# Kernel tuning notes

Measured on AMD Instinct MI355X. Metric: run time of the kernel, lower is better.

The kernel has to match this reference:

```python
import jax, jax.numpy as jnp
import numpy as np

NH = 32      # num_attention_heads
HD = 128     # head dim (kv_channels)
NG = 2       # multi_query_group_num
LAYER_NUMBER = 1


def apply_rotary_pos_emb(x, rope_cache):
    # x: [b, np, sq, hn]; rope_cache: [1, sq_max, rot/2, 2]
    b, nh, sq, hn = x.shape
    rot_dim = rope_cache.shape[-2] * 2
    xr, x_pass = x[..., :rot_dim], x[..., rot_dim:]
    xs = xr.reshape(b, nh, sq, rot_dim // 2, 2)
    c = rope_cache[:, :sq].reshape(-1, 1, sq, rot_dim // 2, 2)
    out = jnp.stack(
        [xs[..., 0] * c[..., 0] - xs[..., 1] * c[..., 1],
         xs[..., 1] * c[..., 0] + xs[..., 0] * c[..., 1]], axis=-1)
    out = out.reshape(b, nh, sq, rot_dim)
    return jnp.concatenate([out, x_pass], axis=-1)


def setup_inputs() -> dict:
    key = jax.random.key(0)
    ks = jax.random.split(key, 5)
    b, sq, h = 2, 2048, 4096
    qkv_out = NH * HD + 2 * NG * HD  # 4608
    return {
        "hidden_states": jax.random.normal(ks[0], (b, sq, h), jnp.float32),
        "rope_cache": jax.random.normal(ks[1], (1, sq, HD // 4, 2), jnp.float32),
        "W_qkv": jax.random.normal(ks[2], (h, qkv_out), jnp.float32) * 0.02,
        "b_qkv": jax.random.normal(ks[3], (qkv_out,), jnp.float32) * 0.02,
        "W_dense": jax.random.normal(ks[4], (NH * HD, h), jnp.float32) * 0.02,
    }


def reference(hidden_states, rope_cache, W_qkv, b_qkv, W_dense):
    b, sq, h = hidden_states.shape
    mixed = hidden_states @ W_qkv + b_qkv  # [b, sq, nh*hd + 2*ng*hd]
    q_sz = NH * HD
    kv_sz = NG * HD
    q = mixed[..., :q_sz].reshape(b, sq, NH, HD).transpose(0, 2, 1, 3)          # [b,nh,sq,hd]
    k = mixed[..., q_sz:q_sz + kv_sz].reshape(b, sq, NG, HD).transpose(0, 2, 1, 3)  # [b,ng,sq,hd]
    v = mixed[..., q_sz + kv_sz:].reshape(b, sq, NG, HD).transpose(0, 2, 1, 3)      # [b,ng,sq,hd]

    q = apply_rotary_pos_emb(q, rope_cache)
    k = apply_rotary_pos_emb(k, rope_cache)

    # expand KV groups to full heads (multi-query attention)
    rep = NH // NG
    k = jnp.broadcast_to(k[:, :, None], (b, NG, rep, sq, HD)).reshape(b, NH, sq, HD)
    v = jnp.broadcast_to(v[:, :, None], (b, NG, rep, sq, HD)).reshape(b, NH, sq, HD)

    # CoreAttention (eager path, fp32 softmax, causal)
    coeff = float(max(1, LAYER_NUMBER))  # apply_query_key_layer_scaling
    norm_factor = np.sqrt(HD) * coeff
    scores = jnp.einsum("bhqd,bhkd->bhqk", q, k) / norm_factor
    scores = scores.astype(jnp.float32) * coeff
    causal = jnp.tril(jnp.ones((sq, sq), dtype=bool))
    scores = jnp.where(causal[None, None], scores, -jnp.inf)
    probs = jax.nn.softmax(scores, axis=-1).astype(v.dtype)
    context = jnp.einsum("bhqk,bhkd->bhqd", probs, v)   # [b,nh,sq,hd]
    context = context.transpose(0, 2, 1, 3).reshape(b, sq, NH * HD)
    return context @ W_dense
```

## Files before the change

kernel.cpp:

```cpp
#include <hip/hip_runtime.h>
#include <hip/hip_bf16.h>
#include <stdint.h>

#define B_    2
#define SQ    2048
#define H_    4096
#define NHEAD 32
#define HDIM  128
#define NGRP  2
#define QKVN  4608
#define SCALE 0.08838834764831845f
#define QSCALE (0.08838834764831845f * 1.4426950408889634f)

typedef __attribute__((ext_vector_type(8))) short bf16x8;
typedef __attribute__((ext_vector_type(4))) short bf16x4;
typedef __attribute__((ext_vector_type(4))) float f32x4;

__device__ __forceinline__ float b2f(short s) {
  union { float f; unsigned u; } x; x.u = ((unsigned)(unsigned short)s) << 16; return x.f;
}
__device__ __forceinline__ short f2b(float f) {
  union { float f; unsigned u; } x; x.f = f;
  unsigned r = x.u + 0x7fffu + ((x.u >> 16) & 1u);
  return (short)(r >> 16);
}
__device__ __forceinline__ void gll16(const void* g, void* l) {
  __builtin_amdgcn_global_load_lds(
      (const __attribute__((address_space(1))) unsigned int*)g,
      (__attribute__((address_space(3))) unsigned int*)l, 16, 0, 0);
}

__global__ void conv_f32_bf16(const float* __restrict__ x, short* __restrict__ y, int n) {
  int i = (blockIdx.x * blockDim.x + threadIdx.x) * 4;
  if (i >= n) return;
  float4 v = *(const float4*)(x + i);
  union { short s[4]; uint2 u; } o;
  o.s[0] = f2b(v.x); o.s[1] = f2b(v.y); o.s[2] = f2b(v.z); o.s[3] = f2b(v.w);
  *(uint2*)(y + i) = o.u;
}

__global__ void transpose_f32_bf16(const float* __restrict__ W, short* __restrict__ Wt,
                                   int R, int C) {
  __shared__ float tile[32][33];
  int c0 = blockIdx.x * 32, r0 = blockIdx.y * 32;
  int tx = threadIdx.x, ty = threadIdx.y;
  #pragma unroll
  for (int i = 0; i < 32; i += 8)
    tile[ty + i][tx] = W[(size_t)(r0 + ty + i) * C + c0 + tx];
  __syncthreads();
  #pragma unroll
  for (int i = 0; i < 32; i += 8)
    Wt[(size_t)(c0 + ty + i) * R + r0 + tx] = f2b(tile[tx][ty + i]);
}

template<bool BIAS, bool OUTF32>
__global__ __launch_bounds__(256, 2) void gemm_bf16(
    const short* __restrict__ A, const short* __restrict__ Bt,
    const float* __restrict__ bias, short* __restrict__ outb,
    float* __restrict__ outf, int M, int N, int K)
{
  __shared__ short smA[128 * 64];
  __shared__ short smB[128 * 64];
  const int t = threadIdx.x;
  const int l = t & 63;
  const int w = t >> 6;
  const int wr = w >> 1, wc = w & 1;
  const int m0 = blockIdx.y * 128, n0 = blockIdx.x * 128;

  const f32x4 z = {0.f, 0.f, 0.f, 0.f};
  f32x4 acc[4][4];
  #pragma unroll
  for (int m = 0; m < 4; ++m)
    #pragma unroll
    for (int n = 0; n < 4; ++n) acc[m][n] = z;

  for (int k0 = 0; k0 < K; k0 += 64) {
    __syncthreads();
    #pragma unroll
    for (int i = 0; i < 4; ++i) {
      int c = t + i * 256;
      int row = c >> 3, slot = c & 7;
      int ss = slot ^ (row & 7);
      gll16(A  + (size_t)(m0 + row) * K + k0 + ss * 8,
            (char*)smA + (i * 256 + w * 64) * 16);
      gll16(Bt + (size_t)(n0 + row) * K + k0 + ss * 8,
            (char*)smB + (i * 256 + w * 64) * 16);
    }
    __syncthreads();
    #pragma unroll
    for (int kk = 0; kk < 2; ++kk) {
      bf16x8 a[4], b[4];
      #pragma unroll
      for (int m = 0; m < 4; ++m) {
        int row = wr * 64 + m * 16 + (l & 15);
        int off = (kk * 64 + ((l >> 4) << 4)) ^ ((row & 7) << 4);
        a[m] = *(const bf16x8*)((const char*)smA + row * 128 + off);
      }
      #pragma unroll
      for (int n = 0; n < 4; ++n) {
        int row = wc * 64 + n * 16 + (l & 15);
        int off = (kk * 64 + ((l >> 4) << 4)) ^ ((row & 7) << 4);
        b[n] = *(const bf16x8*)((const char*)smB + row * 128 + off);
      }
      #pragma unroll
      for (int m = 0; m < 4; ++m)
        #pragma unroll
        for (int n = 0; n < 4; ++n)
          acc[m][n] = __builtin_amdgcn_mfma_f32_16x16x32_bf16(a[m], b[n], acc[m][n], 0, 0, 0);
    }
  }

  #pragma unroll
  for (int m = 0; m < 4; ++m) {
    int row = m0 + wr * 64 + m * 16 + ((l >> 4) << 2);
    #pragma unroll
    for (int n = 0; n < 4; ++n) {
      int col = n0 + wc * 64 + n * 16 + (l & 15);
      float bv = BIAS ? bias[col] : 0.f;
      #pragma unroll
      for (int j = 0; j < 4; ++j) {
        float vv = acc[m][n][j] + bv;
        if (OUTF32) outf[(size_t)(row + j) * N + col] = vv;
        else        outb[(size_t)(row + j) * N + col] = f2b(vv);
      }
    }
  }
}

__global__ __launch_bounds__(512, 2) void gemm256(
    const short* __restrict__ A, const short* __restrict__ Bt,
    float* __restrict__ outf, int M, int N, int K, int nbx)
{
  __shared__ char sm[131072];
  const int t = threadIdx.x, l = t & 63, w = t >> 6;
  const int lq = l & 15, hi = l >> 4;
  const int wm = w >> 2, wn = w & 3;
  const int nwg = (int)gridDim.x;
  const int oid = (int)blockIdx.x;
  const int swz = (oid & 7) * (nwg >> 3) + (oid >> 3);
  const int by = swz / nbx, bx = swz - by * nbx;
  const int m0 = by * 256, n0 = bx * 256;
  const int nkt = K >> 6;

  auto stage = [&](int tt, int u) {
    int kb = (tt < nkt ? tt : tt - nkt) << 6;
    char* buf = sm + ((tt & 1) << 16);
    #pragma unroll
    for (int i = 0; i < 2; ++i) {
      int c = (i << 9) + t;
      int grow = (u < 2) ? (c >> 3) + ((u & 1) << 7)
                         : (c >> 3) + (i << 6) + ((u & 1) << 6);
      int ss = (c & 7) ^ (grow & 7);
      const short* src = (u < 2) ? Bt + (size_t)(n0 + grow) * K + kb + ss * 8
                                 : A  + (size_t)(m0 + grow) * K + kb + ss * 8;
      gll16(src, buf + (u < 2 ? 32768 : 0) + grow * 128 + (c & 7) * 16);
    }
  };

  bf16x8 aC[2][2], bC[4][2];
  auto ldA = [&](int b, int q) {
    #pragma unroll
    for (int fr = 0; fr < 2; ++fr) {
      int ra = wm * 128 + q * 32 + fr * 16 + lq;
      #pragma unroll
      for (int kk = 0; kk < 2; ++kk)
        aC[fr][kk] = *(const bf16x8*)(sm + (b << 16) + ra * 128 + (((kk << 2) + hi) ^ (ra & 7)) * 16);
    }
  };
  auto ldB = [&](int b) {
    #pragma unroll
    for (int fc = 0; fc < 4; ++fc) {
      int rb = wn * 64 + fc * 16 + lq;
      #pragma unroll
      for (int kk = 0; kk < 2; ++kk)
        bC[fc][kk] = *(const bf16x8*)(sm + (b << 16) + 32768 + rb * 128 + (((kk << 2) + hi) ^ (rb & 7)) * 16);
    }
  };

  const f32x4 z = {0.f, 0.f, 0.f, 0.f};
  f32x4 acc[8][4];
  #pragma unroll
  for (int i = 0; i < 8; ++i)
    #pragma unroll
    for (int j = 0; j < 4; ++j) acc[i][j] = z;

  stage(0, 0); stage(0, 1); stage(0, 2); stage(0, 3);
  asm volatile("s_waitcnt vmcnt(0)" ::: "memory");
  __builtin_amdgcn_s_barrier();

#define GPHASE(Q, VM)                                                     \
  {                                                                       \
    if ((Q) == 0) ldB(bsel);                                              \
    ldA(bsel, (Q));                                                       \
    stage(T + 1, (Q));                                                    \
    __builtin_amdgcn_s_barrier();                                         \
    __builtin_amdgcn_s_setprio(1);                                        \
    _Pragma("unroll")                                                     \
    for (int kk = 0; kk < 2; ++kk)                                        \
      _Pragma("unroll")                                                   \
      for (int fr = 0; fr < 2; ++fr)                                      \
        _Pragma("unroll")                                                 \
        for (int fc = 0; fc < 4; ++fc)                                    \
          acc[(Q) * 2 + fr][fc] = __builtin_amdgcn_mfma_f32_16x16x32_bf16(\
              aC[fr][kk], bC[fc][kk], acc[(Q) * 2 + fr][fc], 0, 0, 0);    \
    __builtin_amdgcn_s_setprio(0);                                        \
    if ((VM) == 4) asm volatile("s_waitcnt vmcnt(4)" ::: "memory");       \
    if ((VM) == 2) asm volatile("s_waitcnt vmcnt(2)" ::: "memory");       \
    __builtin_amdgcn_s_barrier();                                         \
  }

  for (int T = 0; T < nkt; ++T) {
    const int bsel = T & 1;
    GPHASE(0, -1)
    GPHASE(1, 4)
    GPHASE(2, -1)
    GPHASE(3, 2)
  }
#undef GPHASE

  #pragma unroll
  for (int q = 0; q < 4; ++q)
    #pragma unroll
    for (int fr = 0; fr < 2; ++fr) {
      int gr0 = m0 + wm * 128 + q * 32 + fr * 16 + hi * 4;
      #pragma unroll
      for (int fc = 0; fc < 4; ++fc) {
        int col = n0 + wn * 64 + fc * 16 + lq;
        #pragma unroll
        for (int j = 0; j < 4; ++j)
          outf[(size_t)(gr0 + j) * N + col] = acc[q * 2 + fr][fc][j];
      }
    }
}

__global__ void rope_split(const short* __restrict__ mixed, const float* __restrict__ rope,
                           short* __restrict__ qo, short* __restrict__ ko, short* __restrict__ vo)
{
  const int CH = QKVN / 8;
  int idx = blockIdx.x * blockDim.x + threadIdx.x;
  if (idx >= B_ * SQ * CH) return;
  int row = idx / CH;
  int cc = (idx - row * CH) * 8;
  int b = row >> 11, s = row & 2047;

  bf16x8 xv = *(const bf16x8*)(mixed + (size_t)row * QKVN + cc);
  float x[8];
  #pragma unroll
  for (int i = 0; i < 8; ++i) x[i] = b2f(xv[i]);

  int sect, hh, d = cc & 127;
  if (cc < 4096)      { sect = 0; hh = cc >> 7; }
  else if (cc < 4352) { sect = 1; hh = (cc - 4096) >> 7; }
  else                { sect = 2; hh = (cc - 4352) >> 7; }

  if (sect < 2 && d < 64) {
    float4 ca = *(const float4*)(rope + s * 64 + d);
    float4 cb = *(const float4*)(rope + s * 64 + d + 4);
    float t0;
    t0 = x[0]*ca.x - x[1]*ca.y; x[1] = x[1]*ca.x + x[0]*ca.y; x[0] = t0;
    t0 = x[2]*ca.z - x[3]*ca.w; x[3] = x[3]*ca.z + x[2]*ca.w; x[2] = t0;
    t0 = x[4]*cb.x - x[5]*cb.y; x[5] = x[5]*cb.x + x[4]*cb.y; x[4] = t0;
    t0 = x[6]*cb.z - x[7]*cb.w; x[7] = x[7]*cb.z + x[6]*cb.w; x[6] = t0;
  }
  if (sect == 0) {
    #pragma unroll
    for (int i = 0; i < 8; ++i) x[i] *= QSCALE;
  }

  short* dst; size_t oidx;
  if (sect == 0)      { dst = qo; oidx = (((size_t)(b * NHEAD + hh) * SQ) + s) * HDIM + d; }
  else if (sect == 1) { dst = ko; oidx = (((size_t)(b * NGRP + hh) * SQ) + s) * HDIM + d; }
  else                { dst = vo; oidx = (((size_t)(b * NGRP + hh) * SQ) + s) * HDIM + d; }
  bf16x8 ov;
  #pragma unroll
  for (int i = 0; i < 8; ++i) ov[i] = f2b(x[i]);
  *(bf16x8*)(dst + oidx) = ov;
}

__global__ __launch_bounds__(512, 2) void attn_fwd(
    const short* __restrict__ q, const short* __restrict__ k,
    const short* __restrict__ v, short* __restrict__ ctx)
{
  __shared__ short smem[8192 + 9216];
  short* smK = smem;
  short* smV = smem + 8192;

  const int h = blockIdx.y, b = blockIdx.z;
  const int g = h >> 4;
  const int t = threadIdx.x, l = t & 63, w = t >> 6;
  const int lq = l & 15, hi = l >> 4;

  const short* qbase = q + ((size_t)(b * NHEAD + h) * SQ) * HDIM;
  const short* kbase = k + ((size_t)(b * NGRP + g) * SQ) * HDIM;
  const short* vbase = v + ((size_t)(b * NGRP + g) * SQ) * HDIM;

  const f32x4 z = {0.f, 0.f, 0.f, 0.f};

  for (int pass = 0; pass < 2; ++pass) {
    const int s = pass ? (7 - (int)blockIdx.x) : (int)blockIdx.x;
    const int q0 = s * 256;
    const int qw = q0 + w * 32;
    const int nkt = 4 * s + 4;

    bf16x8 qf[2][4];
    #pragma unroll
    for (int fq = 0; fq < 2; ++fq)
      #pragma unroll
      for (int kf = 0; kf < 4; ++kf)
        qf[fq][kf] = *(const bf16x8*)(qbase + (size_t)(qw + fq * 16 + lq) * HDIM + kf * 32 + hi * 8);

    f32x4 of[2][8];
    #pragma unroll
    for (int a = 0; a < 2; ++a)
      #pragma unroll
      for (int d = 0; d < 8; ++d) of[a][d] = z;
    float mrow[2] = {-1e30f, -1e30f};
    float lrow[2] = {0.f, 0.f};

    for (int kt = 0; kt < nkt; ++kt) {
      const int kb = kt * 64;
      __syncthreads();
      #pragma unroll
      for (int i = 0; i < 2; ++i) {
        int c = t + i * 512;
        int row = c >> 4, slot = c & 15;
        int ss = slot ^ (row & 7);
        gll16(kbase + (size_t)(kb + row) * HDIM + ss * 8,
              (char*)smK + (i * 512 + w * 64) * 16);
      }
      #pragma unroll
      for (int i = 0; i < 2; ++i) {
        int c = t + i * 512;
        int key = c & 63, d0 = (c >> 6) << 3;
        bf16x8 vv = *(const bf16x8*)(vbase + (size_t)(kb + key) * HDIM + d0);
        #pragma unroll
        for (int jj = 0; jj < 8; ++jj)
          smV[(d0 + jj) * 72 + key] = vv[jj];
      }
      __syncthreads();

      if (kb > qw + 31) continue;

      f32x4 st[2][4];
      #pragma unroll
      for (int fq = 0; fq < 2; ++fq)
        #pragma unroll
        for (int fk = 0; fk < 4; ++fk) st[fq][fk] = z;
      #pragma unroll
      for (int kf = 0; kf < 4; ++kf) {
        bf16x8 kfr[4];
        #pragma unroll
        for (int fk = 0; fk < 4; ++fk) {
          int row = fk * 16 + lq;
          int slot = (kf * 4 + hi) ^ (row & 7);
          kfr[fk] = *(const bf16x8*)((const char*)smK + row * 256 + slot * 16);
        }
        #pragma unroll
        for (int fq = 0; fq < 2; ++fq)
          #pragma unroll
          for (int fk = 0; fk < 4; ++fk)
            st[fq][fk] = __builtin_amdgcn_mfma_f32_16x16x32_bf16(kfr[fk], qf[fq][kf], st[fq][fk], 0, 0, 0);
      }

      bf16x4 pa[2][4];
      #pragma unroll
      for (int fq = 0; fq < 2; ++fq) {
        float sv[16];
        #pragma unroll
        for (int fk = 0; fk < 4; ++fk)
          #pragma unroll
          for (int j = 0; j < 4; ++j) sv[fk * 4 + j] = st[fq][fk][j];
        if (kb + 63 > qw + fq * 16) {
          int qrow = qw + fq * 16 + lq;
          #pragma unroll
          for (int fk = 0; fk < 4; ++fk)
            #pragma unroll
            for (int j = 0; j < 4; ++j)
              if (kb + fk * 16 + hi * 4 + j > qrow) sv[fk * 4 + j] = -1e30f;
        }
        float mx = sv[0];
        #pragma unroll
        for (int i = 1; i < 16; ++i) mx = fmaxf(mx, sv[i]);
        mx = fmaxf(mx, __shfl_xor(mx, 16));
        mx = fmaxf(mx, __shfl_xor(mx, 32));
        if (__any(mx > mrow[fq] + 11.0f)) {
          float mn = fmaxf(mrow[fq], mx);
          float corr = exp2f(mrow[fq] - mn);
          mrow[fq] = mn;
          lrow[fq] *= corr;
          float cj[4];
          #pragma unroll
          for (int j = 0; j < 4; ++j) cj[j] = __shfl(corr, hi * 4 + j);
          #pragma unroll
          for (int df = 0; df < 8; ++df)
            #pragma unroll
            for (int j = 0; j < 4; ++j) of[fq][df][j] *= cj[j];
        }
        float rs = 0.f;
        #pragma unroll
        for (int i = 0; i < 16; ++i) { sv[i] = exp2f(sv[i] - mrow[fq]); rs += sv[i]; }
        rs += __shfl_xor(rs, 16);
        rs += __shfl_xor(rs, 32);
        lrow[fq] += rs;
        #pragma unroll
        for (int fk = 0; fk < 4; ++fk) {
          bf16x4 p;
          p[0] = f2b(sv[fk * 4 + 0]); p[1] = f2b(sv[fk * 4 + 1]);
          p[2] = f2b(sv[fk * 4 + 2]); p[3] = f2b(sv[fk * 4 + 3]);
          pa[fq][fk] = p;
        }
      }

      #pragma unroll
      for (int fk = 0; fk < 4; ++fk) {
        bf16x4 vb[8];
        #pragma unroll
        for (int df = 0; df < 8; ++df)
          vb[df] = *(const bf16x4*)(smV + (df * 16 + lq) * 72 + fk * 16 + hi * 4);
        #pragma unroll
        for (int df = 0; df < 8; ++df) {
          of[0][df] = __builtin_amdgcn_mfma_f32_16x16x16bf16_1k(pa[0][fk], vb[df], of[0][df], 0, 0, 0);
          of[1][df] = __builtin_amdgcn_mfma_f32_16x16x16bf16_1k(pa[1][fk], vb[df], of[1][df], 0, 0, 0);
        }
      }
    }

    #pragma unroll
    for (int fq = 0; fq < 2; ++fq) {
      float inv = 1.f / lrow[fq];
      float ij[4];
      #pragma unroll
      for (int j = 0; j < 4; ++j) ij[j] = __shfl(inv, hi * 4 + j);
      #pragma unroll
      for (int j = 0; j < 4; ++j) {
        int srow = qw + fq * 16 + hi * 4 + j;
        size_t rbase = ((size_t)(b * SQ + srow)) * (NHEAD * HDIM) + (size_t)h * HDIM;
        #pragma unroll
        for (int df = 0; df < 8; ++df)
          ctx[rbase + df * 16 + lq] = f2b(of[fq][df][j] * ij[j]);
      }
    }
    __syncthreads();
  }
}

extern "C" void kernel_launch(void* const* d_in, const int* in_sizes, int n_in,
                              void* d_out, int out_size, void* d_ws, size_t ws_size,
                              hipStream_t stream)
{
  const float* hidden = (const float*)d_in[0];
  const float* rope   = (const float*)d_in[1];
  const float* Wqkv   = (const float*)d_in[2];
  const float* bqkv   = (const float*)d_in[3];
  const float* Wd     = (const float*)d_in[4];
  float* out = (float*)d_out;

  if (ws_size < 113246208ULL) return;
  char* ws = (char*)d_ws;
  short* hsb   = (short*)(ws);
  short* wT    = (short*)(ws + 33554432);
  short* mixed = (short*)(ws + 71303168);
  short* k_r   = (short*)(ws + 109051904);
  short* v_r   = (short*)(ws + 111149056);

  conv_f32_bf16<<<16384, 256, 0, stream>>>(hidden, hsb, B_ * SQ * H_);
  transpose_f32_bf16<<<dim3(QKVN / 32, H_ / 32), dim3(32, 8), 0, stream>>>(Wqkv, wT, H_, QKVN);
  gemm_bf16<true, false><<<dim3(QKVN / 128, (B_ * SQ) / 128), 256, 0, stream>>>(
      hsb, wT, bqkv, mixed, nullptr, B_ * SQ, QKVN, H_);
  rope_split<<<9216, 256, 0, stream>>>(mixed, rope, hsb, k_r, v_r);
  transpose_f32_bf16<<<dim3(H_ / 32, H_ / 32), dim3(32, 8), 0, stream>>>(Wd, wT, H_, H_);
  attn_fwd<<<dim3(4, NHEAD, B_), 512, 0, stream>>>(hsb, k_r, v_r, mixed);
  gemm256<<<256, 512, 0, stream>>>(mixed, wT, out, B_ * SQ, H_, H_, H_ / 256);
}
```

Baseline: 535.5 us.

## Restructure dense GEMM into quadrant phases with deeper prefetch of next tiles

The 256x256 output-projection GEMM is reorganised so each wave computes four 64x32 quadrant sub-tiles. A and B quarter-slabs are staged into LDS in a new order, with loads for the following k-tile issued two phases ahead instead of one. The goal is better overlap of global-to-LDS loads with MFMA work and fewer LDS fragment reloads per phase. It adds an explicit lgkmcnt wait and tighter vmcnt accounting, which carries a risk of stalls or ordering mistakes if the counts do not line up.

```diff
diff --git a/kernel.cpp b/kernel.cpp
--- a/kernel.cpp
+++ b/kernel.cpp
@@ -127,14 +127,14 @@
   }
 }
 
-__global__ __launch_bounds__(512, 2) void gemm256(
+__global__ __launch_bounds__(512, 2) void gemm8ph(
     const short* __restrict__ A, const short* __restrict__ Bt,
     float* __restrict__ outf, int M, int N, int K, int nbx)
 {
   __shared__ char sm[131072];
   const int t = threadIdx.x, l = t & 63, w = t >> 6;
   const int lq = l & 15, hi = l >> 4;
-  const int wm = w >> 2, wn = w & 3;
+  const int wm2 = w >> 2, wn4 = w & 3;
   const int nwg = (int)gridDim.x;
   const int oid = (int)blockIdx.x;
   const int swz = (oid & 7) * (nwg >> 3) + (oid >> 3);
@@ -142,95 +142,101 @@
   const int m0 = by * 256, n0 = bx * 256;
   const int nkt = K >> 6;
 
-  auto stage = [&](int tt, int u) {
-    int kb = (tt < nkt ? tt : tt - nkt) << 6;
-    char* buf = sm + ((tt & 1) << 16);
+  auto stage = [&](int tt, int r) {
+    if (tt >= nkt) return;
+    int kb = tt << 6;
+    const short* base = (r < 2) ? A  + (size_t)(m0 + ((r & 1) << 7)) * K
+                                : Bt + (size_t)(n0 + ((r & 1) << 7)) * K;
+    char* dst = sm + ((tt & 1) << 16) + (r << 14);
     #pragma unroll
     for (int i = 0; i < 2; ++i) {
       int c = (i << 9) + t;
-      int grow = (u < 2) ? (c >> 3) + ((u & 1) << 7)
-                         : (c >> 3) + (i << 6) + ((u & 1) << 6);
-      int ss = (c & 7) ^ (grow & 7);
-      const short* src = (u < 2) ? Bt + (size_t)(n0 + grow) * K + kb + ss * 8
-                                 : A  + (size_t)(m0 + grow) * K + kb + ss * 8;
-      gll16(src, buf + (u < 2 ? 32768 : 0) + grow * 128 + (c & 7) * 16);
+      int row = c >> 3, sl = c & 7;
+      gll16(base + (size_t)row * K + kb + ((sl ^ (row & 7)) << 3), dst + c * 16);
     }
   };
 
-  bf16x8 aC[2][2], bC[4][2];
-  auto ldA = [&](int b, int q) {
-    #pragma unroll
-    for (int fr = 0; fr < 2; ++fr) {
-      int ra = wm * 128 + q * 32 + fr * 16 + lq;
+  bf16x8 aC[4][2], bC[2][2];
+  auto ldA = [&](int bsel, int qa) {
+    #pragma unroll
+    for (int fm = 0; fm < 4; ++fm) {
+      int row = (wm2 << 6) + (fm << 4) + lq;
+      const char* base = sm + (bsel << 16) + (qa << 14) + row * 128;
       #pragma unroll
       for (int kk = 0; kk < 2; ++kk)
-        aC[fr][kk] = *(const bf16x8*)(sm + (b << 16) + ra * 128 + (((kk << 2) + hi) ^ (ra & 7)) * 16);
+        aC[fm][kk] = *(const bf16x8*)(base + ((((kk << 2) + hi) ^ (row & 7)) << 4));
     }
   };
-  auto ldB = [&](int b) {
-    #pragma unroll
-    for (int fc = 0; fc < 4; ++fc) {
-      int rb = wn * 64 + fc * 16 + lq;
+  auto ldB = [&](int bsel, int qb) {
+    #pragma unroll
+    for (int fn = 0; fn < 2; ++fn) {
+      int row = (wn4 << 5) + (fn << 4) + lq;
+      const char* base = sm + (bsel << 16) + 32768 + (qb << 14) + row * 128;
       #pragma unroll
       for (int kk = 0; kk < 2; ++kk)
-        bC[fc][kk] = *(const bf16x8*)(sm + (b << 16) + 32768 + rb * 128 + (((kk << 2) + hi) ^ (rb & 7)) * 16);
+        bC[fn][kk] = *(const bf16x8*)(base + ((((kk << 2) + hi) ^ (row & 7)) << 4));
     }
   };
 
   const f32x4 z = {0.f, 0.f, 0.f, 0.f};
-  f32x4 acc[8][4];
-  #pragma unroll
-  for (int i = 0; i < 8; ++i)
-    #pragma unroll
-    for (int j = 0; j < 4; ++j) acc[i][j] = z;
-
-  stage(0, 0); stage(0, 1); stage(0, 2); stage(0, 3);
-  asm volatile("s_waitcnt vmcnt(0)" ::: "memory");
+  f32x4 acc[4][8];
+  #pragma unroll
+  for (int i = 0; i < 4; ++i)
+    #pragma unroll
+    for (int j = 0; j < 8; ++j) acc[i][j] = z;
+
+  stage(0, 0); stage(0, 2); stage(0, 1); stage(0, 3);
+  stage(1, 0); stage(1, 2);
+  asm volatile("s_waitcnt vmcnt(4)" ::: "memory");
   __builtin_amdgcn_s_barrier();
 
-#define GPHASE(Q, VM)                                                     \
+#define PH(QA, QB, STT, STR, WAIT)                                        \
   {                                                                       \
-    if ((Q) == 0) ldB(bsel);                                              \
-    ldA(bsel, (Q));                                                       \
-    stage(T + 1, (Q));                                                    \
+    if ((QB) == 0) ldA(bsel, (QA));                                       \
+    ldB(bsel, (QB));                                                      \
+    stage((STT), (STR));                                                  \
     __builtin_amdgcn_s_barrier();                                         \
+    asm volatile("s_waitcnt lgkmcnt(0)" ::: "memory");                    \
     __builtin_amdgcn_s_setprio(1);                                        \
     _Pragma("unroll")                                                     \
     for (int kk = 0; kk < 2; ++kk)                                        \
       _Pragma("unroll")                                                   \
-      for (int fr = 0; fr < 2; ++fr)                                      \
+      for (int fm = 0; fm < 4; ++fm)                                      \
         _Pragma("unroll")                                                 \
-        for (int fc = 0; fc < 4; ++fc)                                    \
-          acc[(Q) * 2 + fr][fc] = __builtin_amdgcn_mfma_f32_16x16x32_bf16(\
-              aC[fr][kk], bC[fc][kk], acc[(Q) * 2 + fr][fc], 0, 0, 0);    \
+        for (int fn = 0; fn < 2; ++fn)                                    \
+          acc[((QA) << 1) | (QB)][fm * 2 + fn] =                          \
+              __builtin_amdgcn_mfma_f32_16x16x32_bf16(                    \
+                  aC[fm][kk], bC[fn][kk],                                 \
+                  acc[((QA) << 1) | (QB)][fm * 2 + fn], 0, 0, 0);         \
     __builtin_amdgcn_s_setprio(0);                                        \
-    if ((VM) == 4) asm volatile("s_waitcnt vmcnt(4)" ::: "memory");       \
-    if ((VM) == 2) asm volatile("s_waitcnt vmcnt(2)" ::: "memory");       \
+    if (WAIT) asm volatile("s_waitcnt vmcnt(4)" ::: "memory");            \
     __builtin_amdgcn_s_barrier();                                         \
   }
 
   for (int T = 0; T < nkt; ++T) {
     const int bsel = T & 1;
-    GPHASE(0, -1)
-    GPHASE(1, 4)
-    GPHASE(2, -1)
-    GPHASE(3, 2)
-  }
-#undef GPHASE
-
-  #pragma unroll
-  for (int q = 0; q < 4; ++q)
-    #pragma unroll
-    for (int fr = 0; fr < 2; ++fr) {
-      int gr0 = m0 + wm * 128 + q * 32 + fr * 16 + hi * 4;
-      #pragma unroll
-      for (int fc = 0; fc < 4; ++fc) {
-        int col = n0 + wn * 64 + fc * 16 + lq;
-        #pragma unroll
-        for (int j = 0; j < 4; ++j)
-          outf[(size_t)(gr0 + j) * N + col] = acc[q * 2 + fr][fc][j];
-      }
-    }
+    PH(0, 0, T + 1, 1, 0)
+    PH(0, 1, T + 1, 3, 0)
+    PH(1, 0, T + 2, 0, 0)
+    PH(1, 1, T + 2, 2, 1)
+  }
+#undef PH
+
+  #pragma unroll
+  for (int qa = 0; qa < 2; ++qa)
+    #pragma unroll
+    for (int qb = 0; qb < 2; ++qb)
+      #pragma unroll
+      for (int fm = 0; fm < 4; ++fm) {
+        int r0 = m0 + (qa << 7) + (wm2 << 6) + (fm << 4) + (hi << 2);
+        #pragma unroll
+        for (int fn = 0; fn < 2; ++fn) {
+          int cc = n0 + (qb << 7) + (wn4 << 5) + (fn << 4) + lq;
+          #pragma unroll
+          for (int j = 0; j < 4; ++j)
+            outf[(size_t)(r0 + j) * N + cc] = acc[(qa << 1) | qb][fm * 2 + fn][j];
+        }
+      }
 }
 
 __global__ void rope_split(const short* __restrict__ mixed, const float* __restrict__ rope,
@@ -470,5 +476,5 @@
   rope_split<<<9216, 256, 0, stream>>>(mixed, rope, hsb, k_r, v_r);
   transpose_f32_bf16<<<dim3(H_ / 32, H_ / 32), dim3(32, 8), 0, stream>>>(Wd, wT, H_, H_);
   attn_fwd<<<dim3(4, NHEAD, B_), 512, 0, stream>>>(hsb, k_r, v_r, mixed);
-  gemm256<<<256, 512, 0, stream>>>(mixed, wT, out, B_ * SQ, H_, H_, H_ / 256);
-}
+  gemm8ph<<<256, 512, 0, stream>>>(mixed, wT, out, B_ * SQ, H_, H_, H_ / 256);
+}
```

New measurement: 553.4 us. 1.03x slower.
